# Optimization experiments

Measured on AMD Instinct MI355X. Metric: run time of the kernel, lower is better.

The kernel has to match this reference:

```python
import jax, jax.numpy as jnp
import numpy as np
from jax import lax

HID = 256
BATCH = 256
INPUT_LEN = 512
N_SAMPLES = 16
HORIZON = 64


def _lstm_cell(x, h, c, Wih, Whh, b):
    # x: [B, in], h/c: [B, H]; PyTorch gate order i, f, g, o; b = b_ih + b_hh
    gates = x @ Wih.T + h @ Whh.T + b  # [B, 4H]
    i, f, g, o = jnp.split(gates, 4, axis=-1)
    c_new = jax.nn.sigmoid(f) * c + jax.nn.sigmoid(i) * jnp.tanh(g)
    h_new = jax.nn.sigmoid(o) * jnp.tanh(c_new)
    return h_new, c_new


def setup_inputs() -> dict:
    key = jax.random.key(0)
    ks = jax.random.split(key, 20)
    s = 1.0 / np.sqrt(HID)  # PyTorch LSTM init scale
    def u(k, shape):
        return jax.random.uniform(k, shape, jnp.float32, -s, s)
    inp = {
        "x": jax.random.normal(ks[0], (BATCH, INPUT_LEN), jnp.float32),
        "enc_Wih0": u(ks[1], (4 * HID, 1)),
        "enc_Whh0": u(ks[2], (4 * HID, HID)),
        "enc_b0": u(ks[3], (4 * HID,)),
        "enc_Wih1": u(ks[4], (4 * HID, HID)),
        "enc_Whh1": u(ks[5], (4 * HID, HID)),
        "enc_b1": u(ks[6], (4 * HID,)),
        "dec_Wih0": u(ks[7], (4 * HID, 1)),
        "dec_Whh0": u(ks[8], (4 * HID, HID)),
        "dec_b0": u(ks[9], (4 * HID,)),
        "dec_Wih1": u(ks[10], (4 * HID, HID)),
        "dec_Whh1": u(ks[11], (4 * HID, HID)),
        "dec_b1": u(ks[12], (4 * HID,)),
        "out_W": u(ks[13], (1, HID)),
        "out_b": u(ks[14], (1,)),
        # torch.rand(batch,1,1) per sample -> stacked over n_samples
        "dec_init": jax.random.uniform(ks[15], (N_SAMPLES, BATCH, 1), jnp.float32),
        "horizon": HORIZON,
    }
    return inp


def reference(x, enc_Wih0, enc_Whh0, enc_b0, enc_Wih1, enc_Whh1, enc_b1,
              dec_Wih0, dec_Whh0, dec_b0, dec_Wih1, dec_Whh1, dec_b1,
              out_W, out_b, dec_init, horizon):
    B, T = x.shape
    S = dec_init.shape[0]
    H = enc_Whh0.shape[1]

    # ---- encoder: 2-layer LSTM over input sequence ----
    xs = x.T[:, :, None]  # [T, B, 1]
    zero = jnp.zeros((B, H), x.dtype)

    def enc_step(carry, xt):
        h0, c0, h1, c1 = carry
        h0, c0 = _lstm_cell(xt, h0, c0, enc_Wih0, enc_Whh0, enc_b0)
        h1, c1 = _lstm_cell(h0, h1, c1, enc_Wih1, enc_Whh1, enc_b1)
        return (h0, c0, h1, c1), None

    (h0, c0, h1, c1), _ = lax.scan(enc_step, (zero, zero, zero, zero), xs)

    # ---- decoder: batch the independent n_samples together ----
    def rep(t):  # [B,H] -> [S*B,H]
        return jnp.broadcast_to(t, (S, B, H)).reshape(S * B, H)

    inp0 = dec_init.reshape(S * B, 1)

    def dec_step(carry, _):
        inp, h0, c0, h1, c1 = carry
        h0, c0 = _lstm_cell(inp, h0, c0, dec_Wih0, dec_Whh0, dec_b0)
        h1, c1 = _lstm_cell(h0, h1, c1, dec_Wih1, dec_Whh1, dec_b1)
        pred = h1 @ out_W.T + out_b  # [S*B, 1]
        return (pred, h0, c0, h1, c1), pred

    carry0 = (inp0, rep(h0), rep(c0), rep(h1), rep(c1))
    _, preds = lax.scan(dec_step, carry0, None, length=horizon)
    # preds: [T, S*B, 1] -> [B, S, T]
    return preds[:, :, 0].reshape(horizon, S, B).transpose(2, 1, 0)
```

## Files before the change

kernel.cpp:

```cpp
#include <hip/hip_runtime.h>
#include <stdint.h>


typedef short short8v __attribute__((ext_vector_type(8)));
typedef float float4v __attribute__((ext_vector_type(4)));
typedef unsigned long long u64;
#define MFMA(a,b,c) __builtin_amdgcn_mfma_f32_16x16x32_bf16((a),(b),(c),0,0,0)

#define HIDN 256
#define TLEN 512
#define DB   4096
#define HPE  ((size_t)256 * HIDN)
#define HPD  ((size_t)DB * HIDN)

__device__ __forceinline__ unsigned short f2b(float f) {
    unsigned int u = __float_as_uint(f);
    unsigned int r = ((u >> 16) & 1u) + 0x7FFFu;
    return (unsigned short)((u + r) >> 16);
}
__device__ __forceinline__ float b2f(unsigned short s) {
    return __uint_as_float(((unsigned int)s) << 16);
}
__device__ __forceinline__ float sigf(float x) { return 1.0f / (1.0f + __expf(-x)); }
__device__ __forceinline__ float tanhf2(float x) { return 1.0f - 2.0f / (1.0f + __expf(2.0f * x)); }

__device__ __forceinline__ short8v ld_frag(const unsigned short* p) {
    union { short8v v; u64 q[2]; } u;
    u.q[0] = __hip_atomic_load((const u64*)p,       __ATOMIC_RELAXED, __HIP_MEMORY_SCOPE_AGENT);
    u.q[1] = __hip_atomic_load((const u64*)(p + 4), __ATOMIC_RELAXED, __HIP_MEMORY_SCOPE_AGENT);
    return u.v;
}

__device__ __forceinline__ void hpair_store(unsigned short* buf, int row, int hid,
                                            float h, int lane) {
    unsigned int mine = f2b(h);
    unsigned int part = (unsigned int)__shfl_xor((int)mine, 1);
    if (!(lane & 1)) {
        __hip_atomic_store((unsigned int*)&buf[(size_t)row * HIDN + hid],
                           mine | (part << 16),
                           __ATOMIC_RELAXED, __HIP_MEMORY_SCOPE_AGENT);
    }
}

__device__ __forceinline__ void bar_sync(unsigned int* fl, int slot, unsigned int target,
                                         int lane, int tid, int& dead) {
    __syncthreads();
    if (tid == 0)
        __hip_atomic_store(&fl[slot], target, __ATOMIC_RELAXED, __HIP_MEMORY_SCOPE_AGENT);
    if (!dead) {
        int guard = 0;
        for (;;) {
            unsigned int v = 0xFFFFFFFFu;
            if (lane < 16)
                v = __hip_atomic_load(&fl[lane], __ATOMIC_RELAXED, __HIP_MEMORY_SCOPE_AGENT);
            if (__ballot(v >= target) == ~0ull) break;
            if (++guard > (1 << 20)) { dead = 1; break; }
        }
    }
    __builtin_amdgcn_fence(__ATOMIC_ACQUIRE, "workgroup");
}

__global__ __launch_bounds__(256, 1) void enc_kernel(
    const float* __restrict__ x,
    const float* __restrict__ Wih0, const float* __restrict__ Whh0, const float* __restrict__ b0,
    const float* __restrict__ Wih1, const float* __restrict__ Whh1, const float* __restrict__ b1,
    unsigned short* __restrict__ h0e, unsigned short* __restrict__ h1e,
    unsigned short* __restrict__ finh0, unsigned short* __restrict__ finh1,
    float* __restrict__ finc0, float* __restrict__ finc1,
    unsigned int* __restrict__ flags)
{
    const int tid = threadIdx.x, lane = tid & 63, wv = tid >> 6;
    const int bt = blockIdx.x & 15, hs = blockIdx.x >> 4;
    const int row0 = bt << 4, hidb = hs << 4;
    const int l15 = lane & 15, q = lane >> 4, q8 = q << 3;

    __shared__ float gt[12][16][17];
    __shared__ float xt[16][TLEN + 1];

    for (int idx = tid; idx < 16 * TLEN; idx += 256) {
        int r = idx >> 9, c = idx & 511;
        xt[r][c] = x[(size_t)(row0 + r) * TLEN + c];
    }

    short8v wf[3][8];
    {
        const float* Ws[3] = {Whh0, Wih1, Whh1};
#pragma unroll
        for (int j = 0; j < 3; ++j) {
            int p = wv * 3 + j;
            int mat = p >> 2, g = p & 3;
            const float* rp = Ws[mat] + (size_t)((g << 8) + hidb + l15) * HIDN + q8;
#pragma unroll
            for (int kc = 0; kc < 8; ++kc) {
                short8v v;
#pragma unroll
                for (int i = 0; i < 8; ++i) v[i] = (short)f2b(rp[(kc << 5) + i]);
                wf[j][kc] = v;
            }
        }
    }

    const int erow = tid >> 4, ehid = tid & 15;
    const int grow = row0 + erow, ghid = hidb + ehid;
    float wx[4], bb0v[4], bb1v[4];
#pragma unroll
    for (int g = 0; g < 4; ++g) {
        wx[g]   = Wih0[(g << 8) + ghid];
        bb0v[g] = b0[(g << 8) + ghid];
        bb1v[g] = b1[(g << 8) + ghid];
    }
    float c0 = 0.f, c1 = 0.f;
    unsigned int* fl = flags + (bt << 4);
    int dead = 0;
    const bool useH0 = (wv <= 2), useH1 = (wv >= 2);
    __syncthreads();

    for (int s = 1; s <= 513; ++s) {
        const unsigned short* hr0 = h0e + (size_t)((s - 1) & 1) * HPE;
        const unsigned short* hr1 = h1e + (size_t)((s - 1) & 1) * HPE;
        unsigned short* hw0 = h0e + (size_t)(s & 1) * HPE;
        unsigned short* hw1 = h1e + (size_t)(s & 1) * HPE;

        float4v acc[3] = {{0,0,0,0},{0,0,0,0},{0,0,0,0}};
        short8v a0f[8], a1f[8];
        if (useH0 && s >= 2) {
            const unsigned short* p0 = hr0 + (size_t)(row0 + l15) * HIDN + q8;
#pragma unroll
            for (int kc = 0; kc < 8; ++kc) a0f[kc] = ld_frag(&p0[kc << 5]);
        }
        if (useH1 && s >= 3) {
            const unsigned short* p1 = hr1 + (size_t)(row0 + l15) * HIDN + q8;
#pragma unroll
            for (int kc = 0; kc < 8; ++kc) a1f[kc] = ld_frag(&p1[kc << 5]);
        }
#pragma unroll
        for (int j = 0; j < 3; ++j) {
            int p = wv * 3 + j;
            int mat = p >> 2;
            bool active = (mat == 0) ? (s >= 2 && s <= 512)
                        : (mat == 1) ? (s >= 2)
                                     : (s >= 3);
            if (active) {
                if (mat == 2) {
#pragma unroll
                    for (int kc = 0; kc < 8; ++kc) acc[j] = MFMA(a1f[kc], wf[j][kc], acc[j]);
                } else {
#pragma unroll
                    for (int kc = 0; kc < 8; ++kc) acc[j] = MFMA(a0f[kc], wf[j][kc], acc[j]);
                }
            }
        }
#pragma unroll
        for (int j = 0; j < 3; ++j) {
            int p = wv * 3 + j;
#pragma unroll
            for (int r = 0; r < 4; ++r) gt[p][(q << 2) + r][l15] = acc[j][r];
        }
        __syncthreads();

        if (s <= 512) {
            float xv = xt[erow][s - 1];
            float gi = gt[0][erow][ehid] + wx[0] * xv + bb0v[0];
            float gf = gt[1][erow][ehid] + wx[1] * xv + bb0v[1];
            float gg = gt[2][erow][ehid] + wx[2] * xv + bb0v[2];
            float go = gt[3][erow][ehid] + wx[3] * xv + bb0v[3];
            c0 = sigf(gf) * c0 + sigf(gi) * tanhf2(gg);
            float h0n = sigf(go) * tanhf2(c0);
            hpair_store(hw0, grow, ghid, h0n, lane);
            if (s == 512) {
                finh0[(size_t)grow * HIDN + ghid] = f2b(h0n);
                finc0[(size_t)grow * HIDN + ghid] = c0;
            }
        }
        if (s >= 2) {
            float gi = gt[4][erow][ehid] + gt[8][erow][ehid]  + bb1v[0];
            float gf = gt[5][erow][ehid] + gt[9][erow][ehid]  + bb1v[1];
            float gg = gt[6][erow][ehid] + gt[10][erow][ehid] + bb1v[2];
            float go = gt[7][erow][ehid] + gt[11][erow][ehid] + bb1v[3];
            c1 = sigf(gf) * c1 + sigf(gi) * tanhf2(gg);
            float h1n = sigf(go) * tanhf2(c1);
            hpair_store(hw1, grow, ghid, h1n, lane);
            if (s == 513) {
                finh1[(size_t)grow * HIDN + ghid] = f2b(h1n);
                finc1[(size_t)grow * HIDN + ghid] = c1;
            }
        }
        bar_sync(fl, hs, (unsigned int)s, lane, tid, dead);
    }
}

__global__ __launch_bounds__(256, 1) void dec_kernel(
    const float* __restrict__ Wih0, const float* __restrict__ Whh0, const float* __restrict__ b0,
    const float* __restrict__ Wih1, const float* __restrict__ Whh1, const float* __restrict__ b1,
    const float* __restrict__ outW, const float* __restrict__ outb,
    const float* __restrict__ dinit,
    const unsigned short* __restrict__ finh0, const unsigned short* __restrict__ finh1,
    const float* __restrict__ finc0, const float* __restrict__ finc1,
    unsigned short* __restrict__ h0d, unsigned short* __restrict__ h1d,
    float* __restrict__ out,
    unsigned int* __restrict__ flags)
{
    extern __shared__ unsigned short wlds[];
    const int tid = threadIdx.x, lane = tid & 63, wv = tid >> 6;
    const int bt = blockIdx.x & 15, hs = blockIdx.x >> 4;
    const int row0 = bt << 8, hidb = hs << 4;
    const int l15 = lane & 15, q = lane >> 4, q8 = q << 3;
    const int hid = hidb + l15;

    for (int sl = tid; sl < 6144; sl += 256) {
        int mat = sl >> 11, g = (sl >> 9) & 3, kc = (sl >> 6) & 7, ln = sl & 63;
        const float* W = (mat == 0) ? Whh0 : ((mat == 1) ? Wih1 : Whh1);
        const float* p = W + (size_t)((g << 8) + hidb + (ln & 15)) * HIDN
                           + (kc << 5) + ((ln >> 4) << 3);
        short8v v;
#pragma unroll
        for (int i = 0; i < 8; ++i) v[i] = (short)f2b(p[i]);
        *(short8v*)&wlds[sl << 3] = v;
    }
#define WFRAG(mat, g, kc) (*(const short8v*)&wlds[((((((mat) << 2) + (g)) << 3) + (kc)) << 9) + (lane << 3)])

    float wxd[4], bb0d[4], bb1d[4];
#pragma unroll
    for (int g = 0; g < 4; ++g) {
        wxd[g]  = Wih0[(g << 8) + hid];
        bb0d[g] = b0[(g << 8) + hid];
        bb1d[g] = b1[(g << 8) + hid];
    }
    const float outb_v = outb[0];
    short8v wo8[8];
#pragma unroll
    for (int kc = 0; kc < 8; ++kc)
#pragma unroll
        for (int i = 0; i < 8; ++i) wo8[kc][i] = (short)f2b(outW[(kc << 5) + q8 + i]);

    float c0r[16], c1r[16];
#pragma unroll
    for (int m = 0; m < 4; ++m)
#pragma unroll
        for (int r = 0; r < 4; ++r) {
            int grow = row0 + (wv << 6) + (m << 4) + (q << 2) + r;
            c0r[(m << 2) + r] = finc0[(size_t)(grow & 255) * HIDN + hid];
            c1r[(m << 2) + r] = finc1[(size_t)(grow & 255) * HIDN + hid];
        }

    unsigned int* fl = flags + (bt << 4);
    int dead = 0;
    __syncthreads();

    for (int t = 0; t < 64; ++t) {
        unsigned short* h0wr = h0d + (size_t)(t & 1) * HPD;
        unsigned short* h1wr = h1d + (size_t)(t & 1) * HPD;

        float4v acc1[4][4];
        float predv[4];
        {
            short8v a1f[4][8];
#pragma unroll
            for (int m = 0; m < 4; ++m) {
                int ar = row0 + (wv << 6) + (m << 4) + l15;
                if (t == 0) {
                    const unsigned short* p1 = finh1 + (size_t)(ar & 255) * HIDN + q8;
#pragma unroll
                    for (int kc = 0; kc < 8; ++kc) a1f[m][kc] = *(const short8v*)&p1[kc << 5];
                } else {
                    const unsigned short* p1 = h1d + (size_t)((t - 1) & 1) * HPD
                                                   + (size_t)ar * HIDN + q8;
#pragma unroll
                    for (int kc = 0; kc < 8; ++kc) a1f[m][kc] = ld_frag(&p1[kc << 5]);
                }
            }
#pragma unroll
            for (int m = 0; m < 4; ++m)
#pragma unroll
                for (int g = 0; g < 4; ++g) acc1[m][g] = (float4v){0, 0, 0, 0};
#pragma unroll
            for (int kc = 0; kc < 8; ++kc) {
                short8v w0 = WFRAG(2, 0, kc), w1 = WFRAG(2, 1, kc);
                short8v w2 = WFRAG(2, 2, kc), w3 = WFRAG(2, 3, kc);
#pragma unroll
                for (int m = 0; m < 4; ++m) {
                    acc1[m][0] = MFMA(a1f[m][kc], w0, acc1[m][0]);
                    acc1[m][1] = MFMA(a1f[m][kc], w1, acc1[m][1]);
                    acc1[m][2] = MFMA(a1f[m][kc], w2, acc1[m][2]);
                    acc1[m][3] = MFMA(a1f[m][kc], w3, acc1[m][3]);
                }
            }
#pragma unroll
            for (int m = 0; m < 4; ++m) {
                float pp = 0.f;
#pragma unroll
                for (int kc = 0; kc < 8; ++kc)
#pragma unroll
                    for (int i = 0; i < 8; ++i)
                        pp += b2f((unsigned short)a1f[m][kc][i]) * b2f((unsigned short)wo8[kc][i]);
                pp += __shfl_xor(pp, 16);
                pp += __shfl_xor(pp, 32);
                predv[m] = pp;
            }
        }
        if (hs == 0 && t > 0 && q == 0) {
#pragma unroll
            for (int m = 0; m < 4; ++m) {
                int rg = row0 + (wv << 6) + (m << 4) + l15;
                out[(size_t)(((rg & 255) << 4) + (rg >> 8)) * 64 + (t - 1)] = predv[m] + outb_v;
            }
        }
        {
            short8v a0f[4][8];
#pragma unroll
            for (int m = 0; m < 4; ++m) {
                int ar = row0 + (wv << 6) + (m << 4) + l15;
                if (t == 0) {
                    const unsigned short* p0 = finh0 + (size_t)(ar & 255) * HIDN + q8;
#pragma unroll
                    for (int kc = 0; kc < 8; ++kc) a0f[m][kc] = *(const short8v*)&p0[kc << 5];
                } else {
                    const unsigned short* p0 = h0d + (size_t)((t - 1) & 1) * HPD
                                                   + (size_t)ar * HIDN + q8;
#pragma unroll
                    for (int kc = 0; kc < 8; ++kc) a0f[m][kc] = ld_frag(&p0[kc << 5]);
                }
            }
            float4v acc0[4][4];
#pragma unroll
            for (int m = 0; m < 4; ++m)
#pragma unroll
                for (int g = 0; g < 4; ++g) acc0[m][g] = (float4v){0, 0, 0, 0};
#pragma unroll
            for (int kc = 0; kc < 8; ++kc) {
                short8v w0 = WFRAG(0, 0, kc), w1 = WFRAG(0, 1, kc);
                short8v w2 = WFRAG(0, 2, kc), w3 = WFRAG(0, 3, kc);
#pragma unroll
                for (int m = 0; m < 4; ++m) {
                    acc0[m][0] = MFMA(a0f[m][kc], w0, acc0[m][0]);
                    acc0[m][1] = MFMA(a0f[m][kc], w1, acc0[m][1]);
                    acc0[m][2] = MFMA(a0f[m][kc], w2, acc0[m][2]);
                    acc0[m][3] = MFMA(a0f[m][kc], w3, acc0[m][3]);
                }
            }
#pragma unroll
            for (int m = 0; m < 4; ++m)
#pragma unroll
                for (int r = 0; r < 4; ++r) {
                    int rg = row0 + (wv << 6) + (m << 4) + (q << 2) + r;
                    float inpv = (t == 0) ? dinit[rg]
                                          : (__shfl(predv[m], (q << 2) + r, 64) + outb_v);
                    float gi = acc0[m][0][r] + wxd[0] * inpv + bb0d[0];
                    float gf = acc0[m][1][r] + wxd[1] * inpv + bb0d[1];
                    float gg = acc0[m][2][r] + wxd[2] * inpv + bb0d[2];
                    float go = acc0[m][3][r] + wxd[3] * inpv + bb0d[3];
                    int ci = (m << 2) + r;
                    c0r[ci] = sigf(gf) * c0r[ci] + sigf(gi) * tanhf2(gg);
                    float h0n = sigf(go) * tanhf2(c0r[ci]);
                    hpair_store(h0wr, rg, hid, h0n, lane);
                }
        }
        bar_sync(fl, hs, (unsigned int)(2 * t + 1), lane, tid, dead);

        {
            short8v a0w[4][8];
#pragma unroll
            for (int m = 0; m < 4; ++m) {
                int ar = row0 + (wv << 6) + (m << 4) + l15;
                const unsigned short* p0 = h0wr + (size_t)ar * HIDN + q8;
#pragma unroll
                for (int kc = 0; kc < 8; ++kc) a0w[m][kc] = ld_frag(&p0[kc << 5]);
            }
#pragma unroll
            for (int kc = 0; kc < 8; ++kc) {
                short8v w0 = WFRAG(1, 0, kc), w1 = WFRAG(1, 1, kc);
                short8v w2 = WFRAG(1, 2, kc), w3 = WFRAG(1, 3, kc);
#pragma unroll
                for (int m = 0; m < 4; ++m) {
                    acc1[m][0] = MFMA(a0w[m][kc], w0, acc1[m][0]);
                    acc1[m][1] = MFMA(a0w[m][kc], w1, acc1[m][1]);
                    acc1[m][2] = MFMA(a0w[m][kc], w2, acc1[m][2]);
                    acc1[m][3] = MFMA(a0w[m][kc], w3, acc1[m][3]);
                }
            }
#pragma unroll
            for (int m = 0; m < 4; ++m)
#pragma unroll
                for (int r = 0; r < 4; ++r) {
                    int rg = row0 + (wv << 6) + (m << 4) + (q << 2) + r;
                    float gi = acc1[m][0][r] + bb1d[0];
                    float gf = acc1[m][1][r] + bb1d[1];
                    float gg = acc1[m][2][r] + bb1d[2];
                    float go = acc1[m][3][r] + bb1d[3];
                    int ci = (m << 2) + r;
                    c1r[ci] = sigf(gf) * c1r[ci] + sigf(gi) * tanhf2(gg);
                    float h1n = sigf(go) * tanhf2(c1r[ci]);
                    hpair_store(h1wr, rg, hid, h1n, lane);
                }
        }
        bar_sync(fl, hs, (unsigned int)(2 * t + 2), lane, tid, dead);
    }
    if (hs == 0) {
        const unsigned short* h1f = h1d + HPD;
#pragma unroll
        for (int m = 0; m < 4; ++m) {
            int ar = row0 + (wv << 6) + (m << 4) + l15;
            const unsigned short* p1 = h1f + (size_t)ar * HIDN + q8;
            float pp = 0.f;
#pragma unroll
            for (int kc = 0; kc < 8; ++kc) {
                short8v a1 = ld_frag(&p1[kc << 5]);
#pragma unroll
                for (int i = 0; i < 8; ++i)
                    pp += b2f((unsigned short)a1[i]) * b2f((unsigned short)wo8[kc][i]);
            }
            pp += __shfl_xor(pp, 16);
            pp += __shfl_xor(pp, 32);
            if (q == 0)
                out[(size_t)(((ar & 255) << 4) + (ar >> 8)) * 64 + 63] = pp + outb_v;
        }
    }
}

extern "C" void kernel_launch(void* const* d_in, const int* in_sizes, int n_in,
                              void* d_out, int out_size, void* d_ws, size_t ws_size,
                              hipStream_t stream) {
    (void)in_sizes; (void)n_in; (void)out_size; (void)ws_size;
    const float* x     = (const float*)d_in[0];
    const float* eWih0 = (const float*)d_in[1];
    const float* eWhh0 = (const float*)d_in[2];
    const float* eb0   = (const float*)d_in[3];
    const float* eWih1 = (const float*)d_in[4];
    const float* eWhh1 = (const float*)d_in[5];
    const float* eb1   = (const float*)d_in[6];
    const float* dWih0 = (const float*)d_in[7];
    const float* dWhh0 = (const float*)d_in[8];
    const float* db0   = (const float*)d_in[9];
    const float* dWih1 = (const float*)d_in[10];
    const float* dWhh1 = (const float*)d_in[11];
    const float* db1   = (const float*)d_in[12];
    const float* outW  = (const float*)d_in[13];
    const float* outb  = (const float*)d_in[14];
    const float* dinit = (const float*)d_in[15];

    char* ws = (char*)d_ws;
    unsigned short* h0e   = (unsigned short*)(ws);
    unsigned short* h1e   = (unsigned short*)(ws + 262144);
    unsigned short* h0d   = (unsigned short*)(ws + 524288);
    unsigned short* h1d   = (unsigned short*)(ws + 4718592);
    unsigned short* finh0 = (unsigned short*)(ws + 8912896);
    unsigned short* finh1 = (unsigned short*)(ws + 9043968);
    float* finc0          = (float*)(ws + 9175040);
    float* finc1          = (float*)(ws + 9437184);
    unsigned int* fle     = (unsigned int*)(ws + 9699328);
    unsigned int* fld     = (unsigned int*)(ws + 9700352);

    hipMemsetAsync(ws + 9699328, 0, 2048, stream);
    hipFuncSetAttribute((const void*)dec_kernel,
                        hipFuncAttributeMaxDynamicSharedMemorySize, 98304);
    enc_kernel<<<256, 256, 0, stream>>>(x, eWih0, eWhh0, eb0, eWih1, eWhh1, eb1,
                                        h0e, h1e, finh0, finh1, finc0, finc1, fle);
    dec_kernel<<<256, 256, 98304, stream>>>(dWih0, dWhh0, db0, dWih1, dWhh1, db1,
                                            outW, outb, dinit, finh0, finh1, finc0, finc1,
                                            h0d, h1d, (float*)d_out, fld);
}
```

Before: 4.825 ms.

## Make decoder blocks own full hidden dim for 16 rows, removing grid barriers

The decoder is repartitioned so each block owns 16 batch rows across all 256 hidden units. Hidden state now stays in LDS, and the two cross-block flag barriers per timestep, plus the global h round-trips, disappear. Weights are pre-packed into bf16 MFMA fragment layout by a new pack kernel and streamed from global/L2 each step. The encoder now stages h tiles into LDS with coalesced loads before the MFMA fragment reads. The cost is that every block re-reads the full 1.5 MB of packed weights from cache each step instead of keeping a slice resident in LDS.

```diff
diff --git a/kernel.cpp b/kernel.cpp
--- a/kernel.cpp
+++ b/kernel.cpp
@@ -9,27 +9,15 @@
 
 #define HIDN 256
 #define TLEN 512
-#define DB   4096
 #define HPE  ((size_t)256 * HIDN)
-#define HPD  ((size_t)DB * HIDN)
 
 __device__ __forceinline__ unsigned short f2b(float f) {
     unsigned int u = __float_as_uint(f);
     unsigned int r = ((u >> 16) & 1u) + 0x7FFFu;
     return (unsigned short)((u + r) >> 16);
 }
-__device__ __forceinline__ float b2f(unsigned short s) {
-    return __uint_as_float(((unsigned int)s) << 16);
-}
 __device__ __forceinline__ float sigf(float x) { return 1.0f / (1.0f + __expf(-x)); }
 __device__ __forceinline__ float tanhf2(float x) { return 1.0f - 2.0f / (1.0f + __expf(2.0f * x)); }
-
-__device__ __forceinline__ short8v ld_frag(const unsigned short* p) {
-    union { short8v v; u64 q[2]; } u;
-    u.q[0] = __hip_atomic_load((const u64*)p,       __ATOMIC_RELAXED, __HIP_MEMORY_SCOPE_AGENT);
-    u.q[1] = __hip_atomic_load((const u64*)(p + 4), __ATOMIC_RELAXED, __HIP_MEMORY_SCOPE_AGENT);
-    return u.v;
-}
 
 __device__ __forceinline__ void hpair_store(unsigned short* buf, int row, int hid,
                                             float h, int lane) {
@@ -60,6 +48,24 @@
     __builtin_amdgcn_fence(__ATOMIC_ACQUIRE, "workgroup");
 }
 
+__global__ __launch_bounds__(256) void pack_kernel(
+    const float* __restrict__ Whh0, const float* __restrict__ Wih1,
+    const float* __restrict__ Whh1, unsigned short* __restrict__ pk)
+{
+    int gid = blockIdx.x * 256 + threadIdx.x;
+    int lane = gid & 63;
+    int kc = (gid >> 6) & 7;
+    int n  = (gid >> 9) & 63;
+    int mat = gid >> 15;
+    const float* W = (mat == 0) ? Whh0 : ((mat == 1) ? Wih1 : Whh1);
+    const float* p = W + (size_t)(n * 16 + (lane & 15)) * HIDN
+                       + (kc << 5) + ((lane >> 4) << 3);
+    short8v v;
+#pragma unroll
+    for (int i = 0; i < 8; ++i) v[i] = (short)f2b(p[i]);
+    *(short8v*)&pk[(size_t)gid << 3] = v;
+}
+
 __global__ __launch_bounds__(256, 1) void enc_kernel(
     const float* __restrict__ x,
     const float* __restrict__ Wih0, const float* __restrict__ Whh0, const float* __restrict__ b0,
@@ -76,6 +82,7 @@
 
     __shared__ float gt[12][16][17];
     __shared__ float xt[16][TLEN + 1];
+    __shared__ unsigned short hst0[16][264], hst1[16][264];
 
     for (int idx = tid; idx < 16 * TLEN; idx += 256) {
         int r = idx >> 9, c = idx & 511;
@@ -121,17 +128,37 @@
         unsigned short* hw0 = h0e + (size_t)(s & 1) * HPE;
         unsigned short* hw1 = h1e + (size_t)(s & 1) * HPE;
 
+        if (s >= 2) {
+#pragma unroll
+            for (int k = 0; k < 4; ++k) {
+                int oo = tid + (k << 8);
+                int r = oo >> 6, cu = oo & 63;
+                u64 v = __hip_atomic_load((const u64*)&hr0[(size_t)(row0 + r) * HIDN + (cu << 2)],
+                                          __ATOMIC_RELAXED, __HIP_MEMORY_SCOPE_AGENT);
+                *(u64*)&hst0[r][cu << 2] = v;
+            }
+        }
+        if (s >= 3) {
+#pragma unroll
+            for (int k = 0; k < 4; ++k) {
+                int oo = tid + (k << 8);
+                int r = oo >> 6, cu = oo & 63;
+                u64 v = __hip_atomic_load((const u64*)&hr1[(size_t)(row0 + r) * HIDN + (cu << 2)],
+                                          __ATOMIC_RELAXED, __HIP_MEMORY_SCOPE_AGENT);
+                *(u64*)&hst1[r][cu << 2] = v;
+            }
+        }
+        __syncthreads();
+
         float4v acc[3] = {{0,0,0,0},{0,0,0,0},{0,0,0,0}};
         short8v a0f[8], a1f[8];
         if (useH0 && s >= 2) {
-            const unsigned short* p0 = hr0 + (size_t)(row0 + l15) * HIDN + q8;
-#pragma unroll
-            for (int kc = 0; kc < 8; ++kc) a0f[kc] = ld_frag(&p0[kc << 5]);
+#pragma unroll
+            for (int kc = 0; kc < 8; ++kc) a0f[kc] = *(const short8v*)&hst0[l15][(kc << 5) + q8];
         }
         if (useH1 && s >= 3) {
-            const unsigned short* p1 = hr1 + (size_t)(row0 + l15) * HIDN + q8;
-#pragma unroll
-            for (int kc = 0; kc < 8; ++kc) a1f[kc] = ld_frag(&p1[kc << 5]);
+#pragma unroll
+            for (int kc = 0; kc < 8; ++kc) a1f[kc] = *(const short8v*)&hst1[l15][(kc << 5) + q8];
         }
 #pragma unroll
         for (int j = 0; j < 3; ++j) {
@@ -190,230 +217,167 @@
 }
 
 __global__ __launch_bounds__(256, 1) void dec_kernel(
-    const float* __restrict__ Wih0, const float* __restrict__ Whh0, const float* __restrict__ b0,
-    const float* __restrict__ Wih1, const float* __restrict__ Whh1, const float* __restrict__ b1,
+    const unsigned short* __restrict__ pk,
+    const float* __restrict__ Wih0, const float* __restrict__ b0,
+    const float* __restrict__ b1,
     const float* __restrict__ outW, const float* __restrict__ outb,
     const float* __restrict__ dinit,
     const unsigned short* __restrict__ finh0, const unsigned short* __restrict__ finh1,
     const float* __restrict__ finc0, const float* __restrict__ finc1,
-    unsigned short* __restrict__ h0d, unsigned short* __restrict__ h1d,
-    float* __restrict__ out,
-    unsigned int* __restrict__ flags)
+    float* __restrict__ out)
 {
-    extern __shared__ unsigned short wlds[];
     const int tid = threadIdx.x, lane = tid & 63, wv = tid >> 6;
-    const int bt = blockIdx.x & 15, hs = blockIdx.x >> 4;
-    const int row0 = bt << 8, hidb = hs << 4;
+    const int blk = blockIdx.x;
     const int l15 = lane & 15, q = lane >> 4, q8 = q << 3;
-    const int hid = hidb + l15;
-
-    for (int sl = tid; sl < 6144; sl += 256) {
-        int mat = sl >> 11, g = (sl >> 9) & 3, kc = (sl >> 6) & 7, ln = sl & 63;
-        const float* W = (mat == 0) ? Whh0 : ((mat == 1) ? Wih1 : Whh1);
-        const float* p = W + (size_t)((g << 8) + hidb + (ln & 15)) * HIDN
-                           + (kc << 5) + ((ln >> 4) << 3);
-        short8v v;
-#pragma unroll
-        for (int i = 0; i < 8; ++i) v[i] = (short)f2b(p[i]);
-        *(short8v*)&wlds[sl << 3] = v;
-    }
-#define WFRAG(mat, g, kc) (*(const short8v*)&wlds[((((((mat) << 2) + (g)) << 3) + (kc)) << 9) + (lane << 3)])
-
-    float wxd[4], bb0d[4], bb1d[4];
-#pragma unroll
-    for (int g = 0; g < 4; ++g) {
-        wxd[g]  = Wih0[(g << 8) + hid];
-        bb0d[g] = b0[(g << 8) + hid];
-        bb1d[g] = b1[(g << 8) + hid];
+    const int rbase = blk << 4;
+
+    __shared__ unsigned short hst0[16][264], hst1[16][264];
+    __shared__ float predp[4][16];
+    __shared__ float pr[16];
+
+    float wx[4][4], bv0[4][4], bv1[4][4], ow[4];
+#pragma unroll
+    for (int j = 0; j < 4; ++j) {
+        int hid = (wv << 6) + (j << 4) + l15;
+        ow[j] = outW[hid];
+#pragma unroll
+        for (int ty = 0; ty < 4; ++ty) {
+            wx[ty][j]  = Wih0[(ty << 8) + hid];
+            bv0[ty][j] = b0[(ty << 8) + hid];
+            bv1[ty][j] = b1[(ty << 8) + hid];
+        }
     }
     const float outb_v = outb[0];
-    short8v wo8[8];
-#pragma unroll
-    for (int kc = 0; kc < 8; ++kc)
-#pragma unroll
-        for (int i = 0; i < 8; ++i) wo8[kc][i] = (short)f2b(outW[(kc << 5) + q8 + i]);
-
+
+    short8v h0A[8], h1A[8];
+    {
+        int frow = (rbase + l15) & 255;
+#pragma unroll
+        for (int kc = 0; kc < 8; ++kc) {
+            h0A[kc] = *(const short8v*)&finh0[(size_t)frow * HIDN + (kc << 5) + q8];
+            h1A[kc] = *(const short8v*)&finh1[(size_t)frow * HIDN + (kc << 5) + q8];
+        }
+    }
     float c0r[16], c1r[16];
 #pragma unroll
-    for (int m = 0; m < 4; ++m)
+    for (int j = 0; j < 4; ++j)
 #pragma unroll
         for (int r = 0; r < 4; ++r) {
-            int grow = row0 + (wv << 6) + (m << 4) + (q << 2) + r;
-            c0r[(m << 2) + r] = finc0[(size_t)(grow & 255) * HIDN + hid];
-            c1r[(m << 2) + r] = finc1[(size_t)(grow & 255) * HIDN + hid];
-        }
-
-    unsigned int* fl = flags + (bt << 4);
-    int dead = 0;
+            int hid = (wv << 6) + (j << 4) + l15;
+            int btr = (rbase + (q << 2) + r) & 255;
+            c0r[(j << 2) + r] = finc0[(size_t)btr * HIDN + hid];
+            c1r[(j << 2) + r] = finc1[(size_t)btr * HIDN + hid];
+        }
+    if (tid < 16) pr[tid] = dinit[rbase + tid];
     __syncthreads();
 
+    const int nb = wv << 2;
+
     for (int t = 0; t < 64; ++t) {
-        unsigned short* h0wr = h0d + (size_t)(t & 1) * HPD;
-        unsigned short* h1wr = h1d + (size_t)(t & 1) * HPD;
-
-        float4v acc1[4][4];
-        float predv[4];
-        {
-            short8v a1f[4][8];
-#pragma unroll
-            for (int m = 0; m < 4; ++m) {
-                int ar = row0 + (wv << 6) + (m << 4) + l15;
-                if (t == 0) {
-                    const unsigned short* p1 = finh1 + (size_t)(ar & 255) * HIDN + q8;
-#pragma unroll
-                    for (int kc = 0; kc < 8; ++kc) a1f[m][kc] = *(const short8v*)&p1[kc << 5];
-                } else {
-                    const unsigned short* p1 = h1d + (size_t)((t - 1) & 1) * HPD
-                                                   + (size_t)ar * HIDN + q8;
-#pragma unroll
-                    for (int kc = 0; kc < 8; ++kc) a1f[m][kc] = ld_frag(&p1[kc << 5]);
+        float4v acc[4][4];
+#pragma unroll
+        for (int ty = 0; ty < 4; ++ty)
+#pragma unroll
+            for (int j = 0; j < 4; ++j) acc[ty][j] = (float4v){0, 0, 0, 0};
+#pragma unroll
+        for (int kc = 0; kc < 8; ++kc) {
+#pragma unroll
+            for (int ty = 0; ty < 4; ++ty)
+#pragma unroll
+                for (int j = 0; j < 4; ++j) {
+                    int n = (ty << 4) + nb + j;
+                    short8v bf = *(const short8v*)&pk[(size_t)(((n << 3) + kc) << 9) + (lane << 3)];
+                    acc[ty][j] = MFMA(h0A[kc], bf, acc[ty][j]);
                 }
-            }
-#pragma unroll
-            for (int m = 0; m < 4; ++m)
-#pragma unroll
-                for (int g = 0; g < 4; ++g) acc1[m][g] = (float4v){0, 0, 0, 0};
-#pragma unroll
-            for (int kc = 0; kc < 8; ++kc) {
-                short8v w0 = WFRAG(2, 0, kc), w1 = WFRAG(2, 1, kc);
-                short8v w2 = WFRAG(2, 2, kc), w3 = WFRAG(2, 3, kc);
-#pragma unroll
-                for (int m = 0; m < 4; ++m) {
-                    acc1[m][0] = MFMA(a1f[m][kc], w0, acc1[m][0]);
-                    acc1[m][1] = MFMA(a1f[m][kc], w1, acc1[m][1]);
-                    acc1[m][2] = MFMA(a1f[m][kc], w2, acc1[m][2]);
-                    acc1[m][3] = MFMA(a1f[m][kc], w3, acc1[m][3]);
+        }
+#pragma unroll
+        for (int j = 0; j < 4; ++j)
+#pragma unroll
+            for (int r = 0; r < 4; ++r) {
+                int row = (q << 2) + r;
+                float inp = pr[row];
+                float gi = acc[0][j][r] + wx[0][j] * inp + bv0[0][j];
+                float gf = acc[1][j][r] + wx[1][j] * inp + bv0[1][j];
+                float gg = acc[2][j][r] + wx[2][j] * inp + bv0[2][j];
+                float go = acc[3][j][r] + wx[3][j] * inp + bv0[3][j];
+                int ci = (j << 2) + r;
+                c0r[ci] = sigf(gf) * c0r[ci] + sigf(gi) * tanhf2(gg);
+                float h0n = sigf(go) * tanhf2(c0r[ci]);
+                unsigned int mine = f2b(h0n);
+                unsigned int part = (unsigned int)__shfl_xor((int)mine, 1);
+                if (!(l15 & 1))
+                    *(unsigned int*)&hst0[row][(wv << 6) + (j << 4) + l15] = mine | (part << 16);
+            }
+        __syncthreads();
+#pragma unroll
+        for (int kc = 0; kc < 8; ++kc)
+            h0A[kc] = *(const short8v*)&hst0[l15][(kc << 5) + q8];
+
+        float4v ac1[4][4];
+#pragma unroll
+        for (int ty = 0; ty < 4; ++ty)
+#pragma unroll
+            for (int j = 0; j < 4; ++j) ac1[ty][j] = (float4v){0, 0, 0, 0};
+#pragma unroll
+        for (int kc = 0; kc < 8; ++kc) {
+#pragma unroll
+            for (int ty = 0; ty < 4; ++ty)
+#pragma unroll
+                for (int j = 0; j < 4; ++j) {
+                    int n = (ty << 4) + nb + j;
+                    short8v bf = *(const short8v*)&pk[(size_t)((((64 + n) << 3) + kc) << 9) + (lane << 3)];
+                    ac1[ty][j] = MFMA(h0A[kc], bf, ac1[ty][j]);
                 }
-            }
-#pragma unroll
-            for (int m = 0; m < 4; ++m) {
-                float pp = 0.f;
-#pragma unroll
-                for (int kc = 0; kc < 8; ++kc)
-#pragma unroll
-                    for (int i = 0; i < 8; ++i)
-                        pp += b2f((unsigned short)a1f[m][kc][i]) * b2f((unsigned short)wo8[kc][i]);
-                pp += __shfl_xor(pp, 16);
-                pp += __shfl_xor(pp, 32);
-                predv[m] = pp;
-            }
-        }
-        if (hs == 0 && t > 0 && q == 0) {
-#pragma unroll
-            for (int m = 0; m < 4; ++m) {
-                int rg = row0 + (wv << 6) + (m << 4) + l15;
-                out[(size_t)(((rg & 255) << 4) + (rg >> 8)) * 64 + (t - 1)] = predv[m] + outb_v;
-            }
-        }
-        {
-            short8v a0f[4][8];
-#pragma unroll
-            for (int m = 0; m < 4; ++m) {
-                int ar = row0 + (wv << 6) + (m << 4) + l15;
-                if (t == 0) {
-                    const unsigned short* p0 = finh0 + (size_t)(ar & 255) * HIDN + q8;
-#pragma unroll
-                    for (int kc = 0; kc < 8; ++kc) a0f[m][kc] = *(const short8v*)&p0[kc << 5];
-                } else {
-                    const unsigned short* p0 = h0d + (size_t)((t - 1) & 1) * HPD
-                                                   + (size_t)ar * HIDN + q8;
-#pragma unroll
-                    for (int kc = 0; kc < 8; ++kc) a0f[m][kc] = ld_frag(&p0[kc << 5]);
+        }
+#pragma unroll
+        for (int kc = 0; kc < 8; ++kc) {
+#pragma unroll
+            for (int ty = 0; ty < 4; ++ty)
+#pragma unroll
+                for (int j = 0; j < 4; ++j) {
+                    int n = (ty << 4) + nb + j;
+                    short8v bf = *(const short8v*)&pk[(size_t)((((128 + n) << 3) + kc) << 9) + (lane << 3)];
+                    ac1[ty][j] = MFMA(h1A[kc], bf, ac1[ty][j]);
                 }
-            }
-            float4v acc0[4][4];
-#pragma unroll
-            for (int m = 0; m < 4; ++m)
-#pragma unroll
-                for (int g = 0; g < 4; ++g) acc0[m][g] = (float4v){0, 0, 0, 0};
-#pragma unroll
-            for (int kc = 0; kc < 8; ++kc) {
-                short8v w0 = WFRAG(0, 0, kc), w1 = WFRAG(0, 1, kc);
-                short8v w2 = WFRAG(0, 2, kc), w3 = WFRAG(0, 3, kc);
-#pragma unroll
-                for (int m = 0; m < 4; ++m) {
-                    acc0[m][0] = MFMA(a0f[m][kc], w0, acc0[m][0]);
-                    acc0[m][1] = MFMA(a0f[m][kc], w1, acc0[m][1]);
-                    acc0[m][2] = MFMA(a0f[m][kc], w2, acc0[m][2]);
-                    acc0[m][3] = MFMA(a0f[m][kc], w3, acc0[m][3]);
-                }
-            }
-#pragma unroll
-            for (int m = 0; m < 4; ++m)
-#pragma unroll
-                for (int r = 0; r < 4; ++r) {
-                    int rg = row0 + (wv << 6) + (m << 4) + (q << 2) + r;
-                    float inpv = (t == 0) ? dinit[rg]
-                                          : (__shfl(predv[m], (q << 2) + r, 64) + outb_v);
-                    float gi = acc0[m][0][r] + wxd[0] * inpv + bb0d[0];
-                    float gf = acc0[m][1][r] + wxd[1] * inpv + bb0d[1];
-                    float gg = acc0[m][2][r] + wxd[2] * inpv + bb0d[2];
-                    float go = acc0[m][3][r] + wxd[3] * inpv + bb0d[3];
-                    int ci = (m << 2) + r;
-                    c0r[ci] = sigf(gf) * c0r[ci] + sigf(gi) * tanhf2(gg);
-                    float h0n = sigf(go) * tanhf2(c0r[ci]);
-                    hpair_store(h0wr, rg, hid, h0n, lane);
-                }
-        }
-        bar_sync(fl, hs, (unsigned int)(2 * t + 1), lane, tid, dead);
-
-        {
-            short8v a0w[4][8];
-#pragma unroll
-            for (int m = 0; m < 4; ++m) {
-                int ar = row0 + (wv << 6) + (m << 4) + l15;
-                const unsigned short* p0 = h0wr + (size_t)ar * HIDN + q8;
-#pragma unroll
-                for (int kc = 0; kc < 8; ++kc) a0w[m][kc] = ld_frag(&p0[kc << 5]);
-            }
-#pragma unroll
-            for (int kc = 0; kc < 8; ++kc) {
-                short8v w0 = WFRAG(1, 0, kc), w1 = WFRAG(1, 1, kc);
-                short8v w2 = WFRAG(1, 2, kc), w3 = WFRAG(1, 3, kc);
-#pragma unroll
-                for (int m = 0; m < 4; ++m) {
-                    acc1[m][0] = MFMA(a0w[m][kc], w0, acc1[m][0]);
-                    acc1[m][1] = MFMA(a0w[m][kc], w1, acc1[m][1]);
-                    acc1[m][2] = MFMA(a0w[m][kc], w2, acc1[m][2]);
-                    acc1[m][3] = MFMA(a0w[m][kc], w3, acc1[m][3]);
-                }
-            }
-#pragma unroll
-            for (int m = 0; m < 4; ++m)
-#pragma unroll
-                for (int r = 0; r < 4; ++r) {
-                    int rg = row0 + (wv << 6) + (m << 4) + (q << 2) + r;
-                    float gi = acc1[m][0][r] + bb1d[0];
-                    float gf = acc1[m][1][r] + bb1d[1];
-                    float gg = acc1[m][2][r] + bb1d[2];
-                    float go = acc1[m][3][r] + bb1d[3];
-                    int ci = (m << 2) + r;
-                    c1r[ci] = sigf(gf) * c1r[ci] + sigf(gi) * tanhf2(gg);
-                    float h1n = sigf(go) * tanhf2(c1r[ci]);
-                    hpair_store(h1wr, rg, hid, h1n, lane);
-                }
-        }
-        bar_sync(fl, hs, (unsigned int)(2 * t + 2), lane, tid, dead);
-    }
-    if (hs == 0) {
-        const unsigned short* h1f = h1d + HPD;
-#pragma unroll
-        for (int m = 0; m < 4; ++m) {
-            int ar = row0 + (wv << 6) + (m << 4) + l15;
-            const unsigned short* p1 = h1f + (size_t)ar * HIDN + q8;
-            float pp = 0.f;
-#pragma unroll
-            for (int kc = 0; kc < 8; ++kc) {
-                short8v a1 = ld_frag(&p1[kc << 5]);
-#pragma unroll
-                for (int i = 0; i < 8; ++i)
-                    pp += b2f((unsigned short)a1[i]) * b2f((unsigned short)wo8[kc][i]);
-            }
-            pp += __shfl_xor(pp, 16);
-            pp += __shfl_xor(pp, 32);
-            if (q == 0)
-                out[(size_t)(((ar & 255) << 4) + (ar >> 8)) * 64 + 63] = pp + outb_v;
-        }
+        }
+        float pp[4] = {0.f, 0.f, 0.f, 0.f};
+#pragma unroll
+        for (int j = 0; j < 4; ++j)
+#pragma unroll
+            for (int r = 0; r < 4; ++r) {
+                int row = (q << 2) + r;
+                float gi = ac1[0][j][r] + bv1[0][j];
+                float gf = ac1[1][j][r] + bv1[1][j];
+                float gg = ac1[2][j][r] + bv1[2][j];
+                float go = ac1[3][j][r] + bv1[3][j];
+                int ci = (j << 2) + r;
+                c1r[ci] = sigf(gf) * c1r[ci] + sigf(gi) * tanhf2(gg);
+                float h1n = sigf(go) * tanhf2(c1r[ci]);
+                pp[r] += h1n * ow[j];
+                unsigned int mine = f2b(h1n);
+                unsigned int part = (unsigned int)__shfl_xor((int)mine, 1);
+                if (!(l15 & 1))
+                    *(unsigned int*)&hst1[row][(wv << 6) + (j << 4) + l15] = mine | (part << 16);
+            }
+#pragma unroll
+        for (int off = 1; off < 16; off <<= 1)
+#pragma unroll
+            for (int r = 0; r < 4; ++r) pp[r] += __shfl_xor(pp[r], off);
+        if (l15 == 0) {
+#pragma unroll
+            for (int r = 0; r < 4; ++r) predp[wv][(q << 2) + r] = pp[r];
+        }
+        __syncthreads();
+#pragma unroll
+        for (int kc = 0; kc < 8; ++kc)
+            h1A[kc] = *(const short8v*)&hst1[l15][(kc << 5) + q8];
+        if (tid < 16) {
+            float s = predp[0][tid] + predp[1][tid] + predp[2][tid] + predp[3][tid] + outb_v;
+            pr[tid] = s;
+            int rg = rbase + tid;
+            out[(size_t)(((rg & 255) << 4) + (rg >> 8)) * 64 + t] = s;
+        }
+        __syncthreads();
     }
 }
 
@@ -441,21 +405,17 @@
     char* ws = (char*)d_ws;
     unsigned short* h0e   = (unsigned short*)(ws);
     unsigned short* h1e   = (unsigned short*)(ws + 262144);
-    unsigned short* h0d   = (unsigned short*)(ws + 524288);
-    unsigned short* h1d   = (unsigned short*)(ws + 4718592);
-    unsigned short* finh0 = (unsigned short*)(ws + 8912896);
-    unsigned short* finh1 = (unsigned short*)(ws + 9043968);
-    float* finc0          = (float*)(ws + 9175040);
-    float* finc1          = (float*)(ws + 9437184);
-    unsigned int* fle     = (unsigned int*)(ws + 9699328);
-    unsigned int* fld     = (unsigned int*)(ws + 9700352);
-
-    hipMemsetAsync(ws + 9699328, 0, 2048, stream);
-    hipFuncSetAttribute((const void*)dec_kernel,
-                        hipFuncAttributeMaxDynamicSharedMemorySize, 98304);
+    unsigned short* finh0 = (unsigned short*)(ws + 524288);
+    unsigned short* finh1 = (unsigned short*)(ws + 655360);
+    float* finc0          = (float*)(ws + 786432);
+    float* finc1          = (float*)(ws + 1048576);
+    unsigned int* fle     = (unsigned int*)(ws + 1310720);
+    unsigned short* pk    = (unsigned short*)(ws + 1311744);
+
+    hipMemsetAsync(ws + 1310720, 0, 1024, stream);
+    pack_kernel<<<384, 256, 0, stream>>>(dWhh0, dWih1, dWhh1, pk);
     enc_kernel<<<256, 256, 0, stream>>>(x, eWih0, eWhh0, eb0, eWih1, eWhh1, eb1,
                                         h0e, h1e, finh0, finh1, finc0, finc1, fle);
-    dec_kernel<<<256, 256, 98304, stream>>>(dWih0, dWhh0, db0, dWih1, dWhh1, db1,
-                                            outW, outb, dinit, finh0, finh1, finc0, finc1,
-                                            h0d, h1d, (float*)d_out, fld);
-}
+    dec_kernel<<<256, 256, 0, stream>>>(pk, dWih0, db0, db1, outW, outb, dinit,
+                                        finh0, finh1, finc0, finc1, (float*)d_out);
+}
```

Result: slower. 12.88 ms (+166.9%).
